# Performance work log

Measured on AMD Instinct MI355X. Metric: run time of the kernel, lower is better.

Reference implementation:

```python
import jax, jax.numpy as jnp
import numpy as np
from jax import lax

INT8_NARROW = (-127.0, 127.0)   # brevitas Int8WeightPerTensorFloat (narrow range)
INT8_FULL = (-128.0, 127.0)     # brevitas Int8ActPerTensorFloat
INT32 = (-2.0**31, 2.0**31 - 1)


def _fake_quant(v, scale, qmin, qmax):
    # round-to-nearest, clip, dequant (per-tensor)
    return jnp.clip(jnp.round(v / scale), qmin, qmax) * scale


def _conv(x, w, stride):
    return lax.conv_general_dilated(
        x, w, window_strides=(stride, stride), padding=[(1, 1), (1, 1)],
        dimension_numbers=("NCHW", "OIHW", "NCHW"))


def setup_inputs() -> dict:
    key = jax.random.key(0)
    ks = jax.random.split(key, 5)
    B, Cin, Cout, H = 64, 256, 512, 28
    x = jax.random.normal(ks[0], (B, Cin, H, H), dtype=jnp.float32)
    w1 = jax.random.normal(ks[1], (Cout, Cin, 3, 3), dtype=jnp.float32) * 0.05
    b1 = jax.random.normal(ks[2], (Cout,), dtype=jnp.float32) * 0.01
    w2 = jax.random.normal(ks[3], (Cout, Cout, 3, 3), dtype=jnp.float32) * 0.05
    b2 = jax.random.normal(ks[4], (Cout,), dtype=jnp.float32) * 0.01
    return {
        "x": x, "w1": w1, "b1": b1, "w2": w2, "b2": b2,
        "in_scale": jnp.full((1,), 0.05, dtype=jnp.float32),
        "act1_scale": jnp.full((1,), 0.05, dtype=jnp.float32),
        "act2_scale": jnp.full((1,), 0.05, dtype=jnp.float32),
    }


def reference(x, w1, b1, w2, b2, in_scale, act1_scale, act2_scale):
    s_in = in_scale[0]
    s_a1 = act1_scale[0]
    s_a2 = act2_scale[0]

    # conv1: per-tensor int8 weight fake-quant (max-abs stats, narrow range)
    s_w1 = jnp.max(jnp.abs(w1)) / 127.0
    wq1 = _fake_quant(w1, s_w1, *INT8_NARROW)
    bq1 = _fake_quant(b1, s_in * s_w1, *INT32)  # Int32Bias: scale = in_scale*w_scale
    out = _conv(x, wq1, 2) + bq1[None, :, None, None]

    # act1: int8 activation fake-quant (learned per-tensor scale)
    out = _fake_quant(out, s_a1, *INT8_FULL)

    # conv2
    s_w2 = jnp.max(jnp.abs(w2)) / 127.0
    wq2 = _fake_quant(w2, s_w2, *INT8_NARROW)
    bq2 = _fake_quant(b2, s_a1 * s_w2, *INT32)
    out = _conv(out, wq2, 1) + bq2[None, :, None, None]

    # act2
    out = _fake_quant(out, s_a2, *INT8_FULL)
    return out
```

## Files before the change

### kernel.cpp

```cpp
#include <hip/hip_runtime.h>

typedef int i32x4 __attribute__((ext_vector_type(4)));

__device__ __forceinline__ void gl_lds16(const signed char* g, signed char* l) {
    __builtin_amdgcn_global_load_lds(
        (const __attribute__((address_space(1))) void*)g,
        (__attribute__((address_space(3))) void*)l, 16, 0, 0);
}

#define XQ_SCALE 2048.0f
#define XQ_DELTA (1.0f / 2048.0f)

__device__ __forceinline__ float block_max256(const float* __restrict__ part, int base,
                                              float* __restrict__ sred) {
    float m = part[base + (threadIdx.x & 255)];
#pragma unroll
    for (int off = 32; off > 0; off >>= 1)
        m = fmaxf(m, __shfl_down(m, off));
    __syncthreads();
    if ((threadIdx.x & 63) == 0) sred[threadIdx.x >> 6] = m;
    __syncthreads();
    return fmaxf(fmaxf(sred[0], sred[1]), fmaxf(sred[2], sred[3]));
}

__global__ __launch_bounds__(256) void fused_pre_kernel(
    const float* __restrict__ x,
    const float* __restrict__ w1, const float* __restrict__ w2,
    float* __restrict__ part,
    signed char* __restrict__ xhi, signed char* __restrict__ xlo,
    signed char* __restrict__ act) {
    __shared__ float t[128][33];
    __shared__ float sred[4];
    const int blk = blockIdx.x;
    const int tid = threadIdx.x;
    const uint4 z = {0, 0, 0, 0};

    if (blk < 512) {
        const bool second = blk >= 256;
        const float* w = second ? w2 : w1;
        const int n4 = second ? 589824 : 294912;
        float m = 0.0f;
        for (int i = (blk & 255) * 256 + tid; i < n4; i += 65536) {
            float4 v = ((const float4*)w)[i];
            m = fmaxf(m, fmaxf(fmaxf(fabsf(v.x), fabsf(v.y)), fmaxf(fabsf(v.z), fabsf(v.w))));
        }
#pragma unroll
        for (int off = 32; off > 0; off >>= 1)
            m = fmaxf(m, __shfl_down(m, off));
        if ((tid & 63) == 0) sred[tid >> 6] = m;
        __syncthreads();
        if (tid == 0)
            part[blk] = fmaxf(fmaxf(sred[0], sred[1]), fmaxf(sred[2], sred[3]));
    } else if (blk < 976) {
        const int thr = (blk - 512) * 256 + tid;
        const int b = thr / (116 * 16);
        const int rr = thr - b * (116 * 16);
        const int p = rr >> 4;
        const int ch = rr & 15;
        int h, w;
        if (p < 30)      { h = 0;          w = p; }
        else if (p < 60) { h = 29;         w = p - 30; }
        else if (p < 88) { h = p - 60 + 1; w = 0; }
        else             { h = p - 88 + 1; w = 29; }
        const int off = (b * 900 + h * 30 + w) * 256 + ch * 16;
        *(uint4*)(xhi + off) = z;
        *(uint4*)(xlo + off) = z;
    } else if (blk < 1456) {
        const int thr = (blk - 976) * 256 + tid;
        const int b = thr / (60 * 32);
        const int rr = thr - b * (60 * 32);
        const int p = rr >> 5;
        const int ch = rr & 31;
        int h, w;
        if (p < 16)      { h = 0;          w = p; }
        else if (p < 32) { h = 15;         w = p - 16; }
        else if (p < 46) { h = p - 32 + 1; w = 0; }
        else             { h = p - 46 + 1; w = 15; }
        const int off = (b * 256 + h * 16 + w) * 512 + ch * 16;
        *(uint4*)(act + off) = z;
    } else {
        const int xb = blk - 1456;
        const int hwb = xb % 25;
        const int rest = xb / 25;
        const int cb = rest & 1;
        const int b = rest >> 1;
        const int c0 = cb * 128;
        const int hw0 = hwb * 32;
#pragma unroll
        for (int ci = 0; ci < 16; ++ci) {
            const int crow = (tid >> 5) + ci * 8;
            const int hw = hw0 + (tid & 31);
            float v = 0.0f;
            if (hw < 784) v = x[(b * 256 + c0 + crow) * 784 + hw];
            t[crow][tid & 31] = v;
        }
        __syncthreads();
        const int hw_l = tid >> 3;
        const int cg = (tid & 7) * 16;
        const int hw = hw0 + hw_l;
        if (hw < 784) {
            union { signed char c[16]; uint4 u; } ph, pl;
#pragma unroll
            for (int j = 0; j < 16; ++j) {
                const float v = t[cg + j][hw_l];
                int q = (int)rintf(v * XQ_SCALE);
                q = max(-16383, min(16383, q));
                ph.c[j] = (signed char)(q >> 7);
                pl.c[j] = (signed char)(q & 127);
            }
            const int r = hw / 28;
            const int o = (b * 900 + (r + 1) * 30 + (hw - r * 28) + 1) * 256 + c0 + cg;
            *(uint4*)&xhi[o] = ph.u;
            *(uint4*)&xlo[o] = pl.u;
        }
    }
}

__global__ __launch_bounds__(256) void prep_w_kernel(
    const float* __restrict__ w1, const float* __restrict__ w2,
    const float* __restrict__ b1, const float* __restrict__ b2,
    const float* __restrict__ part,
    const float* __restrict__ in_scale, const float* __restrict__ act1_scale,
    signed char* __restrict__ wq1, signed char* __restrict__ wq2,
    float* __restrict__ bq1, float* __restrict__ bq2,
    float* __restrict__ wmax) {
    __shared__ __align__(16) signed char sw[4608];
    __shared__ float sred[4];
    const int blk = blockIdx.x;
    const int tid = threadIdx.x;

    if (blk < 512) {
        const float inv_s = 127.0f / block_max256(part, 0, sred);
        const int n = blk;
#pragma unroll
        for (int rd = 0; rd < 9; ++rd) {
            const int idx = rd * 256 + tid;
            const float v = w1[n * 2304 + idx];
            float q = rintf(v * inv_s);
            q = fminf(fmaxf(q, -127.0f), 127.0f);
            const int cin = idx / 9;
            const int r = idx - cin * 9;
            sw[r * 256 + cin] = (signed char)(int)q;
        }
        __syncthreads();
        if (tid < 144) *(uint4*)&wq1[n * 2304 + tid * 16] = *(const uint4*)&sw[tid * 16];
    } else if (blk < 1024) {
        const float inv_s = 127.0f / block_max256(part, 256, sred);
        const int n = blk - 512;
#pragma unroll
        for (int rd = 0; rd < 18; ++rd) {
            const int idx = rd * 256 + tid;
            const float v = w2[n * 4608 + idx];
            float q = rintf(v * inv_s);
            q = fminf(fmaxf(q, -127.0f), 127.0f);
            const int cin = idx / 9;
            const int r = idx - cin * 9;
            sw[r * 512 + cin] = (signed char)(int)q;
        }
        __syncthreads();
        for (int o = tid; o < 288; o += 256)
            *(uint4*)&wq2[n * 4608 + o * 16] = *(const uint4*)&sw[o * 16];
    } else {
        const float m1 = block_max256(part, 0, sred);
        const float m2 = block_max256(part, 256, sred);
        if (tid == 0) { wmax[0] = m1; wmax[1] = m2; }
        for (int idx = tid; idx < 1024; idx += 256) {
            if (idx < 512) {
                const float s = (*in_scale) * (m1 * (1.0f / 127.0f));
                float q = rintf(b1[idx] / s);
                q = fminf(fmaxf(q, -2147483648.0f), 2147483648.0f);
                bq1[idx] = q * s;
            } else {
                const int j = idx - 512;
                const float s = (*act1_scale) * (m2 * (1.0f / 127.0f));
                float q = rintf(b2[j] / s);
                q = fminf(fmaxf(q, -2147483648.0f), 2147483648.0f);
                bq2[j] = q * s;
            }
        }
    }
}

template<int CIN, int STRIDE, int HP, int HOUT, bool SPLIT, bool FINAL>
__global__ __launch_bounds__(256, 3) void conv_gemm_kernel(
    const signed char* __restrict__ Ahi,
    const signed char* __restrict__ Alo,
    const signed char* __restrict__ Wt,
    const float* __restrict__ bias,
    const float* __restrict__ wmax,
    const float* __restrict__ s_pre,
    const float* __restrict__ s_act,
    signed char* __restrict__ act_out,
    float* __restrict__ out_final)
{
    constexpr int K = 9 * CIN;
    constexpr int HW = HOUT * HOUT;
    constexpr int NIT = SPLIT ? (K / 128) : (K / 256);
    constexpr int NC = SPLIT ? 8 : 12;
    constexpr int LDSZ = SPLIT ? 32768 : 49152;

    __shared__ __align__(16) signed char smem[LDSZ];

    const int tid = threadIdx.x;
    const int lane = tid & 63;
    const int wv = tid >> 6;
    const int pair = wv >> 1;
    const int nh = wv & 1;
    const int quad = lane >> 4;
    const int l16 = lane & 15;
    const int m0 = blockIdx.y * 64;
    const int n0 = blockIdx.x * 128;

    const int lrow = lane >> 3;
    const int koff = ((lane & 7) ^ lrow) * 16;

    const int kbase = SPLIT ? 0 : pair * (K / 2);

    const signed char* srcb[NC];
    int dsto[NC];
    bool isA[NC];
    if constexpr (SPLIT) {
#pragma unroll
        for (int i = 0; i < NC; ++i) {
            const int g = wv * 8 + i;
            const int type = g >> 3;
            if (type >= 2) {
                const int c = g - 16;
                srcb[i] = Wt + (n0 + c * 8 + lrow) * K + koff;
                dsto[i] = 16384 + c * 1024;
                isA[i] = false;
            } else {
                const int c = g & 7;
                const int m = m0 + c * 8 + lrow;
                const int b = m / HW;
                const int rem = m - b * HW;
                const int oh = rem / HOUT;
                const int ow = rem - oh * HOUT;
                const int off = ((b * HP + oh * STRIDE) * HP + ow * STRIDE) * CIN + koff;
                srcb[i] = (type == 0 ? Ahi : Alo) + off;
                dsto[i] = type * 8192 + c * 1024;
                isA[i] = true;
            }
        }
    } else {
#pragma unroll
        for (int i = 0; i < NC; ++i) {
            const int g = nh * 12 + i;
            if (g < 8) {
                const int c = g;
                const int m = m0 + c * 8 + lrow;
                const int b = m / HW;
                const int rem = m - b * HW;
                const int oh = rem / HOUT;
                const int ow = rem - oh * HOUT;
                const int off = ((b * HP + oh * STRIDE) * HP + ow * STRIDE) * CIN + koff;
                srcb[i] = Ahi + off;
                dsto[i] = pair * 24576 + c * 1024;
                isA[i] = true;
            } else {
                const int c = g - 8;
                srcb[i] = Wt + (n0 + c * 8 + lrow) * K + koff;
                dsto[i] = pair * 24576 + 8192 + c * 1024;
                isA[i] = false;
            }
        }
    }

    const int aoff0 = SPLIT ? (pair * 8192) : (pair * 24576);
    const int boff0 = SPLIT ? 16384 : (pair * 24576 + 8192);

    i32x4 acc[4][4];
#pragma unroll
    for (int mi = 0; mi < 4; ++mi)
#pragma unroll
        for (int ni = 0; ni < 4; ++ni)
            acc[mi][ni] = i32x4{0, 0, 0, 0};

    for (int it = 0; it < NIT; ++it) {
        const int k0 = kbase + it * 128;
        const int r9 = k0 / CIN;
        const int kh = r9 / 3;
        const int kw = r9 - kh * 3;
        const int ashift = (kh * HP + kw) * CIN + (k0 & (CIN - 1));

        __syncthreads();
#pragma unroll
        for (int i = 0; i < NC; ++i)
            gl_lds16(srcb[i] + (isA[i] ? ashift : k0), &smem[dsto[i]]);
        __syncthreads();

#pragma unroll
        for (int ks = 0; ks < 2; ++ks) {
            i32x4 af[4], bfr[4];
#pragma unroll
            for (int mi = 0; mi < 4; ++mi) {
                const int row = mi * 16 + l16;
                const int sl = ((ks * 4 + quad) ^ (row & 7)) * 16;
                af[mi] = *(const i32x4*)&smem[aoff0 + row * 128 + sl];
            }
#pragma unroll
            for (int ni = 0; ni < 4; ++ni) {
                const int row = nh * 64 + ni * 16 + l16;
                const int sl = ((ks * 4 + quad) ^ (row & 7)) * 16;
                bfr[ni] = *(const i32x4*)&smem[boff0 + row * 128 + sl];
            }
#pragma unroll
            for (int mi = 0; mi < 4; ++mi)
#pragma unroll
                for (int ni = 0; ni < 4; ++ni)
                    acc[mi][ni] = __builtin_amdgcn_mfma_i32_16x16x64_i8(af[mi], bfr[ni], acc[mi][ni], 0, 0, 0);
        }
    }

    __syncthreads();
    if (pair == 1) {
#pragma unroll
        for (int mi = 0; mi < 4; ++mi)
#pragma unroll
            for (int ni = 0; ni < 4; ++ni)
                *(i32x4*)&smem[nh * 16384 + (mi * 4 + ni) * 1024 + lane * 16] = acc[mi][ni];
    }
    __syncthreads();
    if (pair == 1) return;

#pragma unroll
    for (int mi = 0; mi < 4; ++mi)
#pragma unroll
        for (int ni = 0; ni < 4; ++ni) {
            const i32x4 other = *(const i32x4*)&smem[nh * 16384 + (mi * 4 + ni) * 1024 + lane * 16];
            if constexpr (SPLIT)
                acc[mi][ni] = acc[mi][ni] * 128 + other;
            else
                acc[mi][ni] = acc[mi][ni] + other;
        }

    float alpha = (*wmax) * (1.0f / 127.0f);
    if (FINAL) alpha *= *s_pre;
    if (SPLIT) alpha *= XQ_DELTA;
    const float sact = *s_act;

    float bv[4];
#pragma unroll
    for (int ni = 0; ni < 4; ++ni)
        bv[ni] = bias[n0 + nh * 64 + ni * 16 + l16];

#pragma unroll
    for (int mi = 0; mi < 4; ++mi) {
#pragma unroll
        for (int i = 0; i < 4; ++i) {
            const int m = m0 + mi * 16 + quad * 4 + i;
            const int b = m / HW;
            const int rem = m - b * HW;
            const int oh = rem / HOUT;
            const int ow = rem - oh * HOUT;
#pragma unroll
            for (int ni = 0; ni < 4; ++ni) {
                const int col = n0 + nh * 64 + ni * 16 + l16;
                const float v = (float)acc[mi][ni][i] * alpha + bv[ni];
                float q = rintf(v / sact);
                q = fminf(fmaxf(q, -128.0f), 127.0f);
                if (FINAL) {
                    out_final[(b * 512 + col) * HW + oh * HOUT + ow] = q * sact;
                } else {
                    act_out[(b * 256 + (oh + 1) * 16 + (ow + 1)) * 512 + col] = (signed char)(int)q;
                }
            }
        }
    }
}

extern "C" void kernel_launch(void* const* d_in, const int* in_sizes, int n_in,
                              void* d_out, int out_size, void* d_ws, size_t ws_size,
                              hipStream_t stream) {
    const float* x  = (const float*)d_in[0];
    const float* w1 = (const float*)d_in[1];
    const float* b1 = (const float*)d_in[2];
    const float* w2 = (const float*)d_in[3];
    const float* b2 = (const float*)d_in[4];
    const float* in_scale   = (const float*)d_in[5];
    const float* act1_scale = (const float*)d_in[6];
    const float* act2_scale = (const float*)d_in[7];
    float* out = (float*)d_out;

    char* ws = (char*)d_ws;
    float* part = (float*)(ws + 0);
    float* wmax = (float*)(ws + 2048);
    float* bq1 = (float*)(ws + 2176);
    float* bq2 = (float*)(ws + 4224);
    signed char* wq1 = (signed char*)(ws + 8192);
    signed char* wq2 = (signed char*)(ws + 1187840);
    signed char* xhi = (signed char*)(ws + 3547136);
    signed char* xlo = (signed char*)(ws + 18292736);
    signed char* act = (signed char*)(ws + 33038336);

    fused_pre_kernel<<<4656, 256, 0, stream>>>(x, w1, w2, part, xhi, xlo, act);

    prep_w_kernel<<<1025, 256, 0, stream>>>(w1, w2, b1, b2, part, in_scale, act1_scale,
                                            wq1, wq2, bq1, bq2, wmax);

    conv_gemm_kernel<256, 2, 30, 14, true, false><<<dim3(4, 196), 256, 0, stream>>>(
        xhi, xlo, wq1, bq1, wmax, act1_scale, act1_scale, act, nullptr);

    conv_gemm_kernel<512, 1, 16, 14, false, true><<<dim3(4, 196), 256, 0, stream>>>(
        act, nullptr, wq2, bq2, wmax + 1, act1_scale, act2_scale, nullptr, out);
}
```

Baseline: 247.2 us.

## Double-buffer LDS staging and drop split-K reduction in non-split conv GEMM

Adds ping-pong LDS buffers so global-to-LDS loads for the next K-slice are issued before computing the current one, replacing the load/sync/compute pattern. For the non-split path, the intra-block split-K over two wave pairs is dropped: all four waves share one K stream and each takes 32 output columns, which removes the LDS reduction epilogue. The split path now needs 64KB of LDS, so its launch bounds drop to 2 blocks per SM. The trade is lower occupancy for the split kernel and a smaller per-wave N tile (less fragment reuse) for the non-split kernel.

```diff
diff --git a/kernel.cpp b/kernel.cpp
--- a/kernel.cpp
+++ b/kernel.cpp
@@ -182,7 +182,7 @@
 }
 
 template<int CIN, int STRIDE, int HP, int HOUT, bool SPLIT, bool FINAL>
-__global__ __launch_bounds__(256, 3) void conv_gemm_kernel(
+__global__ __launch_bounds__(256, SPLIT ? 2 : 3) void conv_gemm_kernel(
     const signed char* __restrict__ Ahi,
     const signed char* __restrict__ Alo,
     const signed char* __restrict__ Wt,
@@ -195,11 +195,12 @@
 {
     constexpr int K = 9 * CIN;
     constexpr int HW = HOUT * HOUT;
-    constexpr int NIT = SPLIT ? (K / 128) : (K / 256);
-    constexpr int NC = SPLIT ? 8 : 12;
-    constexpr int LDSZ = SPLIT ? 32768 : 49152;
-
-    __shared__ __align__(16) signed char smem[LDSZ];
+    constexpr int NIT = K / 128;
+    constexpr int NC = SPLIT ? 8 : 6;
+    constexpr int BUFSZ = SPLIT ? 32768 : 24576;
+    constexpr int NB = SPLIT ? 4 : 2;
+
+    __shared__ __align__(16) signed char smem[2 * BUFSZ];
 
     const int tid = threadIdx.x;
     const int lane = tid & 63;
@@ -213,8 +214,6 @@
 
     const int lrow = lane >> 3;
     const int koff = ((lane & 7) ^ lrow) * 16;
-
-    const int kbase = SPLIT ? 0 : pair * (K / 2);
 
     const signed char* srcb[NC];
     int dsto[NC];
@@ -245,7 +244,7 @@
     } else {
 #pragma unroll
         for (int i = 0; i < NC; ++i) {
-            const int g = nh * 12 + i;
+            const int g = wv * 6 + i;
             if (g < 8) {
                 const int c = g;
                 const int m = m0 + c * 8 + lrow;
@@ -255,94 +254,102 @@
                 const int ow = rem - oh * HOUT;
                 const int off = ((b * HP + oh * STRIDE) * HP + ow * STRIDE) * CIN + koff;
                 srcb[i] = Ahi + off;
-                dsto[i] = pair * 24576 + c * 1024;
+                dsto[i] = c * 1024;
                 isA[i] = true;
             } else {
                 const int c = g - 8;
                 srcb[i] = Wt + (n0 + c * 8 + lrow) * K + koff;
-                dsto[i] = pair * 24576 + 8192 + c * 1024;
+                dsto[i] = 8192 + c * 1024;
                 isA[i] = false;
             }
         }
     }
 
-    const int aoff0 = SPLIT ? (pair * 8192) : (pair * 24576);
-    const int boff0 = SPLIT ? 16384 : (pair * 24576 + 8192);
-
-    i32x4 acc[4][4];
+    const int aoff0 = SPLIT ? (pair * 8192) : 0;
+    const int boff0 = SPLIT ? 16384 : 8192;
+    const int nfix  = SPLIT ? (nh * 64) : (wv * 32);
+
+    i32x4 acc[4][NB];
 #pragma unroll
     for (int mi = 0; mi < 4; ++mi)
 #pragma unroll
-        for (int ni = 0; ni < 4; ++ni)
+        for (int ni = 0; ni < NB; ++ni)
             acc[mi][ni] = i32x4{0, 0, 0, 0};
 
-    for (int it = 0; it < NIT; ++it) {
-        const int k0 = kbase + it * 128;
+    auto STAGE = [&](int bo, int it) {
+        const int k0 = it * 128;
         const int r9 = k0 / CIN;
         const int kh = r9 / 3;
         const int kw = r9 - kh * 3;
         const int ashift = (kh * HP + kw) * CIN + (k0 & (CIN - 1));
-
-        __syncthreads();
 #pragma unroll
         for (int i = 0; i < NC; ++i)
-            gl_lds16(srcb[i] + (isA[i] ? ashift : k0), &smem[dsto[i]]);
-        __syncthreads();
-
+            gl_lds16(srcb[i] + (isA[i] ? ashift : k0), &smem[bo + dsto[i]]);
+    };
+
+    auto COMPUTE = [&](int bo) {
 #pragma unroll
         for (int ks = 0; ks < 2; ++ks) {
-            i32x4 af[4], bfr[4];
+            i32x4 af[4], bfr[NB];
 #pragma unroll
             for (int mi = 0; mi < 4; ++mi) {
                 const int row = mi * 16 + l16;
                 const int sl = ((ks * 4 + quad) ^ (row & 7)) * 16;
-                af[mi] = *(const i32x4*)&smem[aoff0 + row * 128 + sl];
-            }
+                af[mi] = *(const i32x4*)&smem[bo + aoff0 + row * 128 + sl];
+            }
+#pragma unroll
+            for (int ni = 0; ni < NB; ++ni) {
+                const int row = nfix + ni * 16 + l16;
+                const int sl = ((ks * 4 + quad) ^ (row & 7)) * 16;
+                bfr[ni] = *(const i32x4*)&smem[bo + boff0 + row * 128 + sl];
+            }
+#pragma unroll
+            for (int mi = 0; mi < 4; ++mi)
+#pragma unroll
+                for (int ni = 0; ni < NB; ++ni)
+                    acc[mi][ni] = __builtin_amdgcn_mfma_i32_16x16x64_i8(af[mi], bfr[ni], acc[mi][ni], 0, 0, 0);
+        }
+    };
+
+    STAGE(0, 0);
+    __syncthreads();
+    for (int it = 0; it < NIT; it += 2) {
+        if (it + 1 < NIT) STAGE(BUFSZ, it + 1);
+        COMPUTE(0);
+        __syncthreads();
+        if (it + 2 < NIT) STAGE(0, it + 2);
+        COMPUTE(BUFSZ);
+        __syncthreads();
+    }
+
+    if constexpr (SPLIT) {
+        if (pair == 1) {
+#pragma unroll
+            for (int mi = 0; mi < 4; ++mi)
+#pragma unroll
+                for (int ni = 0; ni < 4; ++ni)
+                    *(i32x4*)&smem[nh * 16384 + (mi * 4 + ni) * 1024 + lane * 16] = acc[mi][ni];
+        }
+        __syncthreads();
+        if (pair == 1) return;
+#pragma unroll
+        for (int mi = 0; mi < 4; ++mi)
 #pragma unroll
             for (int ni = 0; ni < 4; ++ni) {
-                const int row = nh * 64 + ni * 16 + l16;
-                const int sl = ((ks * 4 + quad) ^ (row & 7)) * 16;
-                bfr[ni] = *(const i32x4*)&smem[boff0 + row * 128 + sl];
-            }
-#pragma unroll
-            for (int mi = 0; mi < 4; ++mi)
-#pragma unroll
-                for (int ni = 0; ni < 4; ++ni)
-                    acc[mi][ni] = __builtin_amdgcn_mfma_i32_16x16x64_i8(af[mi], bfr[ni], acc[mi][ni], 0, 0, 0);
-        }
-    }
-
-    __syncthreads();
-    if (pair == 1) {
-#pragma unroll
-        for (int mi = 0; mi < 4; ++mi)
-#pragma unroll
-            for (int ni = 0; ni < 4; ++ni)
-                *(i32x4*)&smem[nh * 16384 + (mi * 4 + ni) * 1024 + lane * 16] = acc[mi][ni];
-    }
-    __syncthreads();
-    if (pair == 1) return;
-
-#pragma unroll
-    for (int mi = 0; mi < 4; ++mi)
-#pragma unroll
-        for (int ni = 0; ni < 4; ++ni) {
-            const i32x4 other = *(const i32x4*)&smem[nh * 16384 + (mi * 4 + ni) * 1024 + lane * 16];
-            if constexpr (SPLIT)
+                const i32x4 other = *(const i32x4*)&smem[nh * 16384 + (mi * 4 + ni) * 1024 + lane * 16];
                 acc[mi][ni] = acc[mi][ni] * 128 + other;
-            else
-                acc[mi][ni] = acc[mi][ni] + other;
-        }
+            }
+    }
 
     float alpha = (*wmax) * (1.0f / 127.0f);
     if (FINAL) alpha *= *s_pre;
     if (SPLIT) alpha *= XQ_DELTA;
     const float sact = *s_act;
 
-    float bv[4];
-#pragma unroll
-    for (int ni = 0; ni < 4; ++ni)
-        bv[ni] = bias[n0 + nh * 64 + ni * 16 + l16];
+    float bv[NB];
+#pragma unroll
+    for (int ni = 0; ni < NB; ++ni)
+        bv[ni] = bias[n0 + nfix + ni * 16 + l16];
 
 #pragma unroll
     for (int mi = 0; mi < 4; ++mi) {
@@ -354,8 +361,8 @@
             const int oh = rem / HOUT;
             const int ow = rem - oh * HOUT;
 #pragma unroll
-            for (int ni = 0; ni < 4; ++ni) {
-                const int col = n0 + nh * 64 + ni * 16 + l16;
+            for (int ni = 0; ni < NB; ++ni) {
+                const int col = n0 + nfix + ni * 16 + l16;
                 const float v = (float)acc[mi][ni][i] * alpha + bv[ni];
                 float q = rintf(v / sact);
                 q = fminf(fmaxf(q, -128.0f), 127.0f);
```

Measured after the change: 243.9 us. Within noise of the previous version (-1.4%).
